# Kernel optimization log

Measured on AMD Instinct MI355X. Metric: run time of the kernel, lower is better.

The kernel has to match this reference:

```python
import jax, jax.numpy as jnp
import numpy as np

LN_EPS = 1e-12
BIG = 1e30
BAND = 15  # end index may be at most 15 tokens after start


def output_layer(x, w1, b1, g, b, w2, b2):
    # Linear -> ReLU -> LayerNorm -> Linear (dropout is identity at eval)
    h = jax.nn.relu(x @ w1 + b1)
    mu = jnp.mean(h, axis=-1, keepdims=True)
    var = jnp.mean(jnp.square(h - mu), axis=-1, keepdims=True)
    h = (h - mu) * jax.lax.rsqrt(var + LN_EPS) * g + b
    return h @ w2 + b2


def setup_inputs() -> dict:
    key = jax.random.key(0)
    ks = jax.random.split(key, 8)
    B, S, D = 8, 4096, 1024
    H2 = 2 * D
    inp = {
        "context_input": jax.random.normal(ks[0], (B, S, D), jnp.float32),
        "context_mask": jnp.ones((B, S), jnp.float32),
    }
    def head(k1, k2, n_ans):
        return (
            0.02 * jax.random.normal(k1, (D, H2), jnp.float32),
            jnp.zeros((H2,), jnp.float32),
            jnp.ones((H2,), jnp.float32),
            jnp.zeros((H2,), jnp.float32),
            0.02 * jax.random.normal(k2, (H2, n_ans), jnp.float32),
            jnp.zeros((n_ans,), jnp.float32),
        )
    for name, k1, k2, n_ans in [("start", ks[1], ks[2], 1), ("end", ks[3], ks[4], 1), ("type", ks[5], ks[6], 4)]:
        w1, b1, g, b, w2, b2 = head(k1, k2, n_ans)
        inp[f"{name}_w1"] = w1; inp[f"{name}_b1"] = b1
        inp[f"{name}_g"] = g; inp[f"{name}_b"] = b
        inp[f"{name}_w2"] = w2; inp[f"{name}_b2"] = b2
    return inp


def reference(context_input, context_mask,
              start_w1, start_b1, start_g, start_b, start_w2, start_b2,
              end_w1, end_b1, end_g, end_b, end_w2, end_b2,
              type_w1, type_b1, type_g, type_b, type_w2, type_b2):
    S = context_input.shape[1]
    start_pred = output_layer(context_input, start_w1, start_b1, start_g, start_b, start_w2, start_b2)[..., 0] \
        - BIG * (1.0 - context_mask)  # [B,S]
    end_pred = output_layer(context_input, end_w1, end_b1, end_g, end_b, end_w2, end_b2)[..., 0] \
        - BIG * (1.0 - context_mask)  # [B,S]
    type_pred = output_layer(context_input[:, 0, :], type_w1, type_b1, type_g, type_b, type_w2, type_b2)  # [B,4]

    # outer[b,i,j] = start[b,i] + end[b,j], masked to band 0 <= j-i <= 15
    outer = start_pred[:, :, None] + end_pred[:, None, :]  # [B,S,S]
    i = jnp.arange(S)[:, None]
    j = jnp.arange(S)[None, :]
    band = ((j >= i) & (j <= i + BAND)).astype(outer.dtype)  # [S,S]
    outer = outer - BIG * (1.0 - band)[None]

    yp1 = jnp.argmax(jnp.max(outer, axis=2), axis=1)  # best start index [B]
    yp2 = jnp.argmax(jnp.max(outer, axis=1), axis=1)  # best end index [B]
    return start_pred, end_pred, type_pred, yp1, yp2
```

## Files before the change

kernel.cpp:

```cpp
#include <hip/hip_runtime.h>

typedef _Float16 f16x8 __attribute__((ext_vector_type(8)));
typedef float f32x4 __attribute__((ext_vector_type(4)));

#define BIGF 1e30f
#define M_TOT 32768
#define H2 2048

#define WS_XH 0u
#define WS_WT 67108864u
#define WS_BVEC 75497472u
#define WS_GW2 75513856u
#define WS_CONSTS 75530240u
#define WS_PART 75530496u
#define WS_TPART 100696320u

__global__ void k_convert_x(const float* __restrict__ x, _Float16* __restrict__ xh) {
  size_t i = ((size_t)blockIdx.x * 256 + threadIdx.x) * 8;
  float4 v0 = *(const float4*)(x + i);
  float4 v1 = *(const float4*)(x + i + 4);
  f16x8 h;
  h[0] = (_Float16)v0.x; h[1] = (_Float16)v0.y; h[2] = (_Float16)v0.z; h[3] = (_Float16)v0.w;
  h[4] = (_Float16)v1.x; h[5] = (_Float16)v1.y; h[6] = (_Float16)v1.z; h[7] = (_Float16)v1.w;
  *(f16x8*)(xh + i) = h;
}

__global__ void k_convert_w(const float* __restrict__ w_s, const float* __restrict__ w_e,
                            _Float16* __restrict__ wt) {
  __shared__ float tile[64][65];
  const float* w = blockIdx.z ? w_e : w_s;
  int n0 = blockIdx.x * 64, k0 = blockIdx.y * 64;
  int tx = threadIdx.x & 63, ty = threadIdx.x >> 6;
#pragma unroll
  for (int i = ty; i < 64; i += 4) tile[i][tx] = w[(size_t)(k0 + i) * H2 + n0 + tx];
  __syncthreads();
#pragma unroll
  for (int i = ty; i < 64; i += 4) {
    wt[((size_t)(blockIdx.z * H2 + n0 + i)) * 1024 + k0 + tx] = (_Float16)tile[tx][i];
  }
}

__global__ void k_pack(const float* __restrict__ s_b1, const float* __restrict__ s_g,
                       const float* __restrict__ s_w2, const float* __restrict__ e_b1,
                       const float* __restrict__ e_g, const float* __restrict__ e_w2,
                       float* __restrict__ bvec, float* __restrict__ gw2) {
  int i = blockIdx.x * 256 + threadIdx.x;
  int head = i >> 11, j = i & (H2 - 1);
  bvec[i] = head ? e_b1[j] : s_b1[j];
  gw2[i] = head ? e_g[j] * e_w2[j] : s_g[j] * s_w2[j];
}

__global__ void k_consts(const float* __restrict__ s_g, const float* __restrict__ s_b,
                         const float* __restrict__ s_w2, const float* __restrict__ s_b2,
                         const float* __restrict__ e_g, const float* __restrict__ e_b,
                         const float* __restrict__ e_w2, const float* __restrict__ e_b2,
                         float* __restrict__ consts) {
  int h = blockIdx.x;
  const float* g = h ? e_g : s_g;
  const float* b = h ? e_b : s_b;
  const float* w2 = h ? e_w2 : s_w2;
  const float* b2 = h ? e_b2 : s_b2;
  float c1 = 0.f, c2 = 0.f;
  for (int j = threadIdx.x; j < H2; j += 256) {
    float w = w2[j];
    c1 += g[j] * w;
    c2 += b[j] * w;
  }
  for (int m = 1; m < 64; m <<= 1) { c1 += __shfl_xor(c1, m); c2 += __shfl_xor(c2, m); }
  __shared__ float r1[4], r2[4];
  int wid = threadIdx.x >> 6;
  if ((threadIdx.x & 63) == 0) { r1[wid] = c1; r2[wid] = c2; }
  __syncthreads();
  if (threadIdx.x == 0) {
    consts[h * 2 + 0] = r1[0] + r1[1] + r1[2] + r1[3];
    consts[h * 2 + 1] = r2[0] + r2[1] + r2[2] + r2[3] + b2[0];
  }
}

#define BUF 65536
#define STA(q, tile, bufo)                                                              \
  __builtin_amdgcn_global_load_lds(                                                     \
      (const __attribute__((address_space(1))) unsigned int*)(srcA + (size_t)(q) * 131072 + (size_t)(tile) * 128), \
      (__attribute__((address_space(3))) unsigned int*)(lds + (bufo) + (q) * 8192 + t * 16), 16, 0, 0)
#define STB(q, tile, bufo)                                                              \
  __builtin_amdgcn_global_load_lds(                                                     \
      (const __attribute__((address_space(1))) unsigned int*)(srcB + (size_t)(q) * 131072 + (size_t)(tile) * 128), \
      (__attribute__((address_space(3))) unsigned int*)(lds + (bufo) + 32768 + (q) * 8192 + t * 16), 16, 0, 0)
#define RDA(mi, low) (*(const f16x8*)(lds + ob + arow + (mi) * 2048 + (low)))
#define RDB(nj, low) (*(const f16x8*)(lds + ob + brow + (nj) * 2048 + (low)))
#define PHASE_MFMA(m0, m1, a00, a10, a01, a11)                                          \
  do {                                                                                  \
    __builtin_amdgcn_s_setprio(1);                                                      \
    _Pragma("unroll")                                                                   \
    for (int nj = 0; nj < 4; ++nj) {                                                    \
      acc[m0][nj] = __builtin_amdgcn_mfma_f32_16x16x32_f16(a00, bf[nj][0], acc[m0][nj], 0, 0, 0); \
      acc[m1][nj] = __builtin_amdgcn_mfma_f32_16x16x32_f16(a10, bf[nj][0], acc[m1][nj], 0, 0, 0); \
    }                                                                                   \
    _Pragma("unroll")                                                                   \
    for (int nj = 0; nj < 4; ++nj) {                                                    \
      acc[m0][nj] = __builtin_amdgcn_mfma_f32_16x16x32_f16(a01, bf[nj][1], acc[m0][nj], 0, 0, 0); \
      acc[m1][nj] = __builtin_amdgcn_mfma_f32_16x16x32_f16(a11, bf[nj][1], acc[m1][nj], 0, 0, 0); \
    }                                                                                   \
    __builtin_amdgcn_s_setprio(0);                                                      \
  } while (0)

__global__ __launch_bounds__(512, 2) void k_gemm(const _Float16* __restrict__ Xh,
                                                 const _Float16* __restrict__ Wt,
                                                 const float* __restrict__ bvec,
                                                 const float* __restrict__ gw2,
                                                 float* __restrict__ partials) {
  __shared__ char lds[2 * BUF];
  const int nb = blockIdx.x;
  const int mb = blockIdx.y;
  const int t = threadIdx.x;
  const int lane = t & 63, wid = t >> 6;
  const int c15 = lane & 15, g4 = lane >> 4;
  const int wmg = wid >> 2;
  const int wn = (wid & 3) * 64;

  f32x4 acc[8][4];
#pragma unroll
  for (int i = 0; i < 8; ++i)
#pragma unroll
    for (int j = 0; j < 4; ++j) acc[i][j] = (f32x4){0.f, 0.f, 0.f, 0.f};

  const char* Abase = (const char*)(Xh + (size_t)mb * 256 * 1024);
  const char* Bbase = (const char*)(Wt + (size_t)nb * 256 * 1024);
  const int rowl = t >> 3;
  const int swz = ((t & 7) * 16) ^ ((rowl & 7) << 4);
  const char* srcA = Abase + (size_t)rowl * 2048 + swz;
  const char* srcB = Bbase + (size_t)rowl * 2048 + swz;

  const int xorv = (c15 & 7) << 4;
  const int low0 = (g4 * 16) ^ xorv;
  const int low1 = (64 + g4 * 16) ^ xorv;
  const int arow = (wmg * 128 + c15) * 128;
  const int brow = 32768 + (wn + c15) * 128;

  STA(0, 0, 0); STA(1, 0, 0); STA(2, 0, 0); STA(3, 0, 0);
  STB(0, 0, 0); STB(1, 0, 0); STB(2, 0, 0); STB(3, 0, 0);
  STB(0, 1, BUF); STB(1, 1, BUF); STB(2, 1, BUF); STB(3, 1, BUF);
  STA(0, 1, BUF); STA(2, 1, BUF);

  unsigned ob = 0;
#pragma unroll 2
  for (int g = 0; g < 16; ++g) {
    unsigned onext = ob ^ BUF;
    if (g + 1 < 16) { STA(1, g + 1, onext); STA(3, g + 1, onext); }
    if (g < 15) asm volatile("s_waitcnt vmcnt(8)" ::: "memory");
    else        asm volatile("s_waitcnt vmcnt(0)" ::: "memory");
    __builtin_amdgcn_s_barrier();
    asm volatile("" ::: "memory");
    __builtin_amdgcn_sched_barrier(0);

    f16x8 bf[4][2];
#pragma unroll
    for (int nj = 0; nj < 4; ++nj) {
      bf[nj][0] = RDB(nj, low0);
      bf[nj][1] = RDB(nj, low1);
    }
    {
      f16x8 a00 = RDA(0, low0), a01 = RDA(0, low1);
      f16x8 a10 = RDA(1, low0), a11 = RDA(1, low1);
      PHASE_MFMA(0, 1, a00, a10, a01, a11);
    }
    __builtin_amdgcn_s_barrier();

    {
      f16x8 a00 = RDA(2, low0), a01 = RDA(2, low1);
      f16x8 a10 = RDA(3, low0), a11 = RDA(3, low1);
      if (g + 2 < 16) { STB(0, g + 2, ob); STB(1, g + 2, ob); }
      PHASE_MFMA(2, 3, a00, a10, a01, a11);
    }
    __builtin_amdgcn_s_barrier();

    {
      f16x8 a00 = RDA(4, low0), a01 = RDA(4, low1);
      f16x8 a10 = RDA(5, low0), a11 = RDA(5, low1);
      if (g + 2 < 16) { STB(2, g + 2, ob); STB(3, g + 2, ob); }
      PHASE_MFMA(4, 5, a00, a10, a01, a11);
    }
    __builtin_amdgcn_s_barrier();

    {
      f16x8 a00 = RDA(6, low0), a01 = RDA(6, low1);
      f16x8 a10 = RDA(7, low0), a11 = RDA(7, low1);
      if (g + 2 < 16) { STA(0, g + 2, ob); STA(2, g + 2, ob); }
      PHASE_MFMA(6, 7, a00, a10, a01, a11);
    }
    __builtin_amdgcn_s_barrier();

    ob = onext;
  }

  float bv[4], gv[4];
#pragma unroll
  for (int nj = 0; nj < 4; ++nj) {
    int col = nb * 256 + wn + nj * 16 + c15;
    bv[nj] = bvec[col];
    gv[nj] = gw2[col];
  }
  const int slice = nb * 4 + (wid & 3);
#pragma unroll
  for (int mi = 0; mi < 8; ++mi) {
#pragma unroll
    for (int r = 0; r < 4; ++r) {
      float s1 = 0.f, s2 = 0.f, s3 = 0.f;
#pragma unroll
      for (int nj = 0; nj < 4; ++nj) {
        float v = acc[mi][nj][r] + bv[nj];
        v = fmaxf(v, 0.f);
        s1 += v;
        s2 += v * v;
        s3 += v * gv[nj];
      }
#pragma unroll
      for (int m = 1; m < 16; m <<= 1) {
        s1 += __shfl_xor(s1, m);
        s2 += __shfl_xor(s2, m);
        s3 += __shfl_xor(s3, m);
      }
      if (c15 == 0) {
        int rowg = mb * 256 + wmg * 128 + mi * 16 + g4 * 4 + r;
        partials[((size_t)(slice * 3 + 0)) * M_TOT + rowg] = s1;
        partials[((size_t)(slice * 3 + 1)) * M_TOT + rowg] = s2;
        partials[((size_t)(slice * 3 + 2)) * M_TOT + rowg] = s3;
      }
    }
  }
}

__global__ void k_reduce(const float* __restrict__ partials, const float* __restrict__ consts,
                         const float* __restrict__ mask, float* __restrict__ out) {
  int m = blockIdx.x * 256 + threadIdx.x;
  float s1 = 0.f, s2 = 0.f, s3 = 0.f, e1 = 0.f, e2 = 0.f, e3 = 0.f;
  for (int nb2 = 0; nb2 < 32; ++nb2) {
    s1 += partials[((size_t)(nb2 * 3 + 0)) * M_TOT + m];
    s2 += partials[((size_t)(nb2 * 3 + 1)) * M_TOT + m];
    s3 += partials[((size_t)(nb2 * 3 + 2)) * M_TOT + m];
  }
  for (int nb2 = 32; nb2 < 64; ++nb2) {
    e1 += partials[((size_t)(nb2 * 3 + 0)) * M_TOT + m];
    e2 += partials[((size_t)(nb2 * 3 + 1)) * M_TOT + m];
    e3 += partials[((size_t)(nb2 * 3 + 2)) * M_TOT + m];
  }
  const float H = (float)H2;
  float mu = s1 / H;
  float var = fmaxf(s2 / H - mu * mu, 0.f);
  float rs = 1.f / sqrtf(var + 1e-12f);
  float score_s = rs * (s3 - mu * consts[0]) + consts[1];
  mu = e1 / H;
  var = fmaxf(e2 / H - mu * mu, 0.f);
  rs = 1.f / sqrtf(var + 1e-12f);
  float score_e = rs * (e3 - mu * consts[2]) + consts[3];
  float mk = BIGF * (1.f - mask[m]);
  out[m] = score_s - mk;
  out[M_TOT + m] = score_e - mk;
}

__global__ void k_type_partial(const float* __restrict__ X, const float* __restrict__ w1,
                               const float* __restrict__ b1, const float* __restrict__ g,
                               const float* __restrict__ w2, float* __restrict__ tpart) {
  __shared__ float xs[1024];
  int cb = blockIdx.x, tok = blockIdx.y, t = threadIdx.x;
  const float* xp = X + (size_t)tok * 4096 * 1024;
  for (int i = t; i < 1024; i += 256) xs[i] = xp[i];
  __syncthreads();
  int j = cb * 256 + t;
  float dot = 0.f;
  for (int k = 0; k < 1024; ++k) dot += xs[k] * w1[(size_t)k * H2 + j];
  float h = fmaxf(dot + b1[j], 0.f);
  float gj = g[j];
  float s[6];
  s[0] = h;
  s[1] = h * h;
#pragma unroll
  for (int c = 0; c < 4; ++c) s[2 + c] = h * gj * w2[j * 4 + c];
  for (int m = 1; m < 64; m <<= 1)
#pragma unroll
    for (int q = 0; q < 6; ++q) s[q] += __shfl_xor(s[q], m);
  __shared__ float red[4][6];
  int wid = t >> 6;
  if ((t & 63) == 0)
#pragma unroll
    for (int q = 0; q < 6; ++q) red[wid][q] = s[q];
  __syncthreads();
  if (t == 0)
#pragma unroll
    for (int q = 0; q < 6; ++q)
      tpart[(tok * 8 + cb) * 6 + q] = red[0][q] + red[1][q] + red[2][q] + red[3][q];
}

__global__ void k_type_final(const float* __restrict__ tpart, const float* __restrict__ g,
                             const float* __restrict__ bb, const float* __restrict__ w2,
                             const float* __restrict__ b2, float* __restrict__ out) {
  int t = threadIdx.x;
  float c1[4] = {0.f, 0.f, 0.f, 0.f}, c2[4] = {0.f, 0.f, 0.f, 0.f};
  for (int j = t; j < H2; j += 256) {
    float gj = g[j], bj = bb[j];
#pragma unroll
    for (int c = 0; c < 4; ++c) {
      float w = w2[j * 4 + c];
      c1[c] += gj * w;
      c2[c] += bj * w;
    }
  }
  for (int m = 1; m < 64; m <<= 1)
#pragma unroll
    for (int c = 0; c < 4; ++c) { c1[c] += __shfl_xor(c1[c], m); c2[c] += __shfl_xor(c2[c], m); }
  __shared__ float rC1[4][4], rC2[4][4];
  int wid = t >> 6;
  if ((t & 63) == 0)
#pragma unroll
    for (int c = 0; c < 4; ++c) { rC1[wid][c] = c1[c]; rC2[wid][c] = c2[c]; }
  __syncthreads();
  __shared__ float sC1[4], sC2[4];
  if (t < 4) {
    sC1[t] = rC1[0][t] + rC1[1][t] + rC1[2][t] + rC1[3][t];
    sC2[t] = rC2[0][t] + rC2[1][t] + rC2[2][t] + rC2[3][t];
  }
  __syncthreads();
  if (t < 32) {
    int tok = t >> 2, c = t & 3;
    float s1 = 0.f, s2 = 0.f, s3 = 0.f;
    for (int cb = 0; cb < 8; ++cb) {
      s1 += tpart[(tok * 8 + cb) * 6 + 0];
      s2 += tpart[(tok * 8 + cb) * 6 + 1];
      s3 += tpart[(tok * 8 + cb) * 6 + 2 + c];
    }
    float mu = s1 / (float)H2;
    float var = fmaxf(s2 / (float)H2 - mu * mu, 0.f);
    float rs = 1.f / sqrtf(var + 1e-12f);
    out[65536 + tok * 4 + c] = rs * (s3 - mu * sC1[c]) + sC2[c] + b2[c];
  }
}

__global__ void k_band(const float* __restrict__ preds, float* __restrict__ out) {
  __shared__ float ss[4096], se[4096];
  int b = blockIdx.x, t = threadIdx.x;
  for (int i = t; i < 4096; i += 256) {
    ss[i] = preds[(size_t)b * 4096 + i];
    se[i] = preds[M_TOT + (size_t)b * 4096 + i];
  }
  __syncthreads();
  float bv1 = -3.0e38f, bv2 = -3.0e38f;
  int bi1 = 0x7fffffff, bi2 = 0x7fffffff;
  for (int i = t; i < 4096; i += 256) {
    float m1 = -3.0e38f;
    int jmax = i + 15 < 4095 ? i + 15 : 4095;
    for (int j = i; j <= jmax; ++j) m1 = fmaxf(m1, se[j]);
    float v1 = ss[i] + m1;
    if (v1 > bv1 || (v1 == bv1 && i < bi1)) { bv1 = v1; bi1 = i; }
    float m2 = -3.0e38f;
    int imin = i - 15 > 0 ? i - 15 : 0;
    for (int j = imin; j <= i; ++j) m2 = fmaxf(m2, ss[j]);
    float v2 = se[i] + m2;
    if (v2 > bv2 || (v2 == bv2 && i < bi2)) { bv2 = v2; bi2 = i; }
  }
  for (int m = 1; m < 64; m <<= 1) {
    float ov = __shfl_xor(bv1, m);
    int oi = __shfl_xor(bi1, m);
    if (ov > bv1 || (ov == bv1 && oi < bi1)) { bv1 = ov; bi1 = oi; }
    ov = __shfl_xor(bv2, m);
    oi = __shfl_xor(bi2, m);
    if (ov > bv2 || (ov == bv2 && oi < bi2)) { bv2 = ov; bi2 = oi; }
  }
  __shared__ float rv[2][4];
  __shared__ int ri[2][4];
  int wid = t >> 6;
  if ((t & 63) == 0) { rv[0][wid] = bv1; ri[0][wid] = bi1; rv[1][wid] = bv2; ri[1][wid] = bi2; }
  __syncthreads();
  if (t == 0) {
    float v = rv[0][0];
    int ix = ri[0][0];
    for (int w = 1; w < 4; ++w)
      if (rv[0][w] > v || (rv[0][w] == v && ri[0][w] < ix)) { v = rv[0][w]; ix = ri[0][w]; }
    out[65568 + b] = (float)ix;
    v = rv[1][0];
    ix = ri[1][0];
    for (int w = 1; w < 4; ++w)
      if (rv[1][w] > v || (rv[1][w] == v && ri[1][w] < ix)) { v = rv[1][w]; ix = ri[1][w]; }
    out[65576 + b] = (float)ix;
  }
}

extern "C" void kernel_launch(void* const* d_in, const int* in_sizes, int n_in, void* d_out,
                              int out_size, void* d_ws, size_t ws_size, hipStream_t stream) {
  const float* X = (const float*)d_in[0];
  const float* mask = (const float*)d_in[1];
  const float* s_w1 = (const float*)d_in[2];
  const float* s_b1 = (const float*)d_in[3];
  const float* s_g = (const float*)d_in[4];
  const float* s_b = (const float*)d_in[5];
  const float* s_w2 = (const float*)d_in[6];
  const float* s_b2 = (const float*)d_in[7];
  const float* e_w1 = (const float*)d_in[8];
  const float* e_b1 = (const float*)d_in[9];
  const float* e_g = (const float*)d_in[10];
  const float* e_b = (const float*)d_in[11];
  const float* e_w2 = (const float*)d_in[12];
  const float* e_b2 = (const float*)d_in[13];
  const float* t_w1 = (const float*)d_in[14];
  const float* t_b1 = (const float*)d_in[15];
  const float* t_g = (const float*)d_in[16];
  const float* t_b = (const float*)d_in[17];
  const float* t_w2 = (const float*)d_in[18];
  const float* t_b2 = (const float*)d_in[19];

  char* ws = (char*)d_ws;
  _Float16* Xh = (_Float16*)(ws + WS_XH);
  _Float16* Wt = (_Float16*)(ws + WS_WT);
  float* bvec = (float*)(ws + WS_BVEC);
  float* gw2 = (float*)(ws + WS_GW2);
  float* consts = (float*)(ws + WS_CONSTS);
  float* partials = (float*)(ws + WS_PART);
  float* tpart = (float*)(ws + WS_TPART);
  float* out = (float*)d_out;

  k_convert_x<<<16384, 256, 0, stream>>>(X, Xh);
  k_convert_w<<<dim3(32, 16, 2), 256, 0, stream>>>(s_w1, e_w1, Wt);
  k_pack<<<16, 256, 0, stream>>>(s_b1, s_g, s_w2, e_b1, e_g, e_w2, bvec, gw2);
  k_consts<<<2, 256, 0, stream>>>(s_g, s_b, s_w2, s_b2, e_g, e_b, e_w2, e_b2, consts);
  k_gemm<<<dim3(16, 128), 512, 0, stream>>>(Xh, Wt, bvec, gw2, partials);
  k_reduce<<<128, 256, 0, stream>>>(partials, consts, mask, out);
  k_type_partial<<<dim3(8, 8), 256, 0, stream>>>(X, t_w1, t_b1, t_g, t_w2, tpart);
  k_type_final<<<1, 256, 0, stream>>>(tpart, t_g, t_b, t_w2, t_b2, out);
  k_band<<<8, 256, 0, stream>>>(out, out);
}
```

Before: 427.3 us.

## Software-pipeline LDS fragment reads ahead of MFMA phases in GEMM main loop

Restructures the k-loop so each phase issues the LDS reads for the next A fragments (and, at the end, the next tile's B and first A fragments) before running the current phase's MFMAs. Fine-grained lgkmcnt waits replace whole-phase waits, and the loop is fully unrolled with ping-pong register fragment sets. The aim is to hide LDS read latency behind matrix-core work. In exchange it raises register pressure under the 2-waves-per-SIMD launch bound, and the hand-tuned vmcnt/lgkmcnt counts must stay exactly right to remain correct.

```diff
diff --git a/kernel.cpp b/kernel.cpp
--- a/kernel.cpp
+++ b/kernel.cpp
@@ -86,23 +86,72 @@
   __builtin_amdgcn_global_load_lds(                                                     \
       (const __attribute__((address_space(1))) unsigned int*)(srcB + (size_t)(q) * 131072 + (size_t)(tile) * 128), \
       (__attribute__((address_space(3))) unsigned int*)(lds + (bufo) + 32768 + (q) * 8192 + t * 16), 16, 0, 0)
-#define RDA(mi, low) (*(const f16x8*)(lds + ob + arow + (mi) * 2048 + (low)))
-#define RDB(nj, low) (*(const f16x8*)(lds + ob + brow + (nj) * 2048 + (low)))
-#define PHASE_MFMA(m0, m1, a00, a10, a01, a11)                                          \
-  do {                                                                                  \
-    __builtin_amdgcn_s_setprio(1);                                                      \
-    _Pragma("unroll")                                                                   \
-    for (int nj = 0; nj < 4; ++nj) {                                                    \
-      acc[m0][nj] = __builtin_amdgcn_mfma_f32_16x16x32_f16(a00, bf[nj][0], acc[m0][nj], 0, 0, 0); \
-      acc[m1][nj] = __builtin_amdgcn_mfma_f32_16x16x32_f16(a10, bf[nj][0], acc[m1][nj], 0, 0, 0); \
+
+#define READA(AF, mi0, BUFO)                                                            \
+  AF[0][0] = *(const f16x8*)(lds + (BUFO) + arow + (mi0) * 2048 + low0);                \
+  AF[0][1] = *(const f16x8*)(lds + (BUFO) + arow + (mi0) * 2048 + low1);                \
+  AF[1][0] = *(const f16x8*)(lds + (BUFO) + arow + ((mi0) + 1) * 2048 + low0);          \
+  AF[1][1] = *(const f16x8*)(lds + (BUFO) + arow + ((mi0) + 1) * 2048 + low1);
+
+#define READB(BF, BUFO)                                                                 \
+  _Pragma("unroll")                                                                     \
+  for (int nj = 0; nj < 4; ++nj) {                                                      \
+    BF[nj][0] = *(const f16x8*)(lds + (BUFO) + brow + nj * 2048 + low0);                \
+    BF[nj][1] = *(const f16x8*)(lds + (BUFO) + brow + nj * 2048 + low1);                \
+  }
+
+#define MFMA2(m0, m1, AF, BF)                                                           \
+  __builtin_amdgcn_s_setprio(1);                                                        \
+  _Pragma("unroll")                                                                     \
+  for (int nj = 0; nj < 4; ++nj) {                                                      \
+    acc[m0][nj] = __builtin_amdgcn_mfma_f32_16x16x32_f16(AF[0][0], BF[nj][0], acc[m0][nj], 0, 0, 0); \
+    acc[m1][nj] = __builtin_amdgcn_mfma_f32_16x16x32_f16(AF[1][0], BF[nj][0], acc[m1][nj], 0, 0, 0); \
+  }                                                                                     \
+  _Pragma("unroll")                                                                     \
+  for (int nj = 0; nj < 4; ++nj) {                                                      \
+    acc[m0][nj] = __builtin_amdgcn_mfma_f32_16x16x32_f16(AF[0][1], BF[nj][1], acc[m0][nj], 0, 0, 0); \
+    acc[m1][nj] = __builtin_amdgcn_mfma_f32_16x16x32_f16(AF[1][1], BF[nj][1], acc[m1][nj], 0, 0, 0); \
+  }                                                                                     \
+  __builtin_amdgcn_s_setprio(0);
+
+#define K_ITER(g, OB, OBN, BFC, BFN)                                                    \
+  {                                                                                     \
+                           \
+    READA(afB, 2, OB);                                                                  \
+    if ((g) < 15) { STA(1, (g) + 1, OBN); STA(3, (g) + 1, OBN); }                       \
+    asm volatile("s_waitcnt lgkmcnt(4)" ::: "memory");                                  \
+    __builtin_amdgcn_s_barrier();                                                       \
+    __builtin_amdgcn_sched_barrier(0);                                                  \
+    MFMA2(0, 1, afA, BFC);                                                              \
+                           \
+    READA(afA, 4, OB);                                                                  \
+    if ((g) < 14) { STB(0, (g) + 2, OB); STB(1, (g) + 2, OB); }                         \
+    asm volatile("s_waitcnt lgkmcnt(4)" ::: "memory");                                  \
+    __builtin_amdgcn_s_barrier();                                                       \
+    __builtin_amdgcn_sched_barrier(0);                                                  \
+    MFMA2(2, 3, afB, BFC);                                                              \
+           \
+    READA(afB, 6, OB);                                                                  \
+    if ((g) < 14) { STB(2, (g) + 2, OB); STB(3, (g) + 2, OB); }                         \
+    if ((g) < 14)       asm volatile("s_waitcnt vmcnt(4)" ::: "memory");                \
+    else if ((g) == 14) asm volatile("s_waitcnt vmcnt(0)" ::: "memory");                \
+    asm volatile("s_waitcnt lgkmcnt(4)" ::: "memory");                                  \
+    __builtin_amdgcn_s_barrier();                                                       \
+    __builtin_amdgcn_sched_barrier(0);                                                  \
+    MFMA2(4, 5, afA, BFC);                                                              \
+       \
+    if ((g) < 15) {                                                                     \
+      READB(BFN, OBN);                                                                  \
+      READA(afA, 0, OBN);                                                               \
+      if ((g) < 14) { STA(0, (g) + 2, OB); STA(2, (g) + 2, OB); }                       \
+      asm volatile("s_waitcnt lgkmcnt(12)" ::: "memory");                               \
+    } else {                                                                            \
+      asm volatile("s_waitcnt lgkmcnt(0)" ::: "memory");                                \
     }                                                                                   \
-    _Pragma("unroll")                                                                   \
-    for (int nj = 0; nj < 4; ++nj) {                                                    \
-      acc[m0][nj] = __builtin_amdgcn_mfma_f32_16x16x32_f16(a01, bf[nj][1], acc[m0][nj], 0, 0, 0); \
-      acc[m1][nj] = __builtin_amdgcn_mfma_f32_16x16x32_f16(a11, bf[nj][1], acc[m1][nj], 0, 0, 0); \
-    }                                                                                   \
-    __builtin_amdgcn_s_setprio(0);                                                      \
-  } while (0)
+    __builtin_amdgcn_s_barrier();                                                       \
+    __builtin_amdgcn_sched_barrier(0);                                                  \
+    MFMA2(6, 7, afB, BFC);                                                              \
+  }
 
 __global__ __launch_bounds__(512, 2) void k_gemm(const _Float16* __restrict__ Xh,
                                                  const _Float16* __restrict__ Wt,
@@ -141,56 +190,18 @@
   STB(0, 0, 0); STB(1, 0, 0); STB(2, 0, 0); STB(3, 0, 0);
   STB(0, 1, BUF); STB(1, 1, BUF); STB(2, 1, BUF); STB(3, 1, BUF);
   STA(0, 1, BUF); STA(2, 1, BUF);
-
-  unsigned ob = 0;
-#pragma unroll 2
-  for (int g = 0; g < 16; ++g) {
-    unsigned onext = ob ^ BUF;
-    if (g + 1 < 16) { STA(1, g + 1, onext); STA(3, g + 1, onext); }
-    if (g < 15) asm volatile("s_waitcnt vmcnt(8)" ::: "memory");
-    else        asm volatile("s_waitcnt vmcnt(0)" ::: "memory");
-    __builtin_amdgcn_s_barrier();
-    asm volatile("" ::: "memory");
-    __builtin_amdgcn_sched_barrier(0);
-
-    f16x8 bf[4][2];
-#pragma unroll
-    for (int nj = 0; nj < 4; ++nj) {
-      bf[nj][0] = RDB(nj, low0);
-      bf[nj][1] = RDB(nj, low1);
-    }
-    {
-      f16x8 a00 = RDA(0, low0), a01 = RDA(0, low1);
-      f16x8 a10 = RDA(1, low0), a11 = RDA(1, low1);
-      PHASE_MFMA(0, 1, a00, a10, a01, a11);
-    }
-    __builtin_amdgcn_s_barrier();
-
-    {
-      f16x8 a00 = RDA(2, low0), a01 = RDA(2, low1);
-      f16x8 a10 = RDA(3, low0), a11 = RDA(3, low1);
-      if (g + 2 < 16) { STB(0, g + 2, ob); STB(1, g + 2, ob); }
-      PHASE_MFMA(2, 3, a00, a10, a01, a11);
-    }
-    __builtin_amdgcn_s_barrier();
-
-    {
-      f16x8 a00 = RDA(4, low0), a01 = RDA(4, low1);
-      f16x8 a10 = RDA(5, low0), a11 = RDA(5, low1);
-      if (g + 2 < 16) { STB(2, g + 2, ob); STB(3, g + 2, ob); }
-      PHASE_MFMA(4, 5, a00, a10, a01, a11);
-    }
-    __builtin_amdgcn_s_barrier();
-
-    {
-      f16x8 a00 = RDA(6, low0), a01 = RDA(6, low1);
-      f16x8 a10 = RDA(7, low0), a11 = RDA(7, low1);
-      if (g + 2 < 16) { STA(0, g + 2, ob); STA(2, g + 2, ob); }
-      PHASE_MFMA(6, 7, a00, a10, a01, a11);
-    }
-    __builtin_amdgcn_s_barrier();
-
-    ob = onext;
+  asm volatile("s_waitcnt vmcnt(6)" ::: "memory");
+  __builtin_amdgcn_s_barrier();
+  __builtin_amdgcn_sched_barrier(0);
+
+  f16x8 afA[2][2], afB[2][2], bfA[4][2], bfB[4][2];
+  READB(bfA, 0);
+  READA(afA, 0, 0);
+
+#pragma unroll
+  for (int gp = 0; gp < 8; ++gp) {
+    K_ITER(2 * gp, 0u, BUF, bfA, bfB);
+    K_ITER(2 * gp + 1, BUF, 0u, bfB, bfA);
   }
 
   float bv[4], gv[4];
```

Measured after the change: 428.9 us. About the same (+0.4%).
